# Optimization experiments

Hardware: AMD Instinct MI355X
Metric: run time of the kernel (lower is better)

## Reference

```python
import jax, jax.numpy as jnp
import numpy as np

B, S, CACHE, HID, NH, NKV, HD, INTER = 2, 1024, 2048, 2048, 8, 1, 256, 16384
EPS = 1e-6
SOFTCAP = 50.0
SCALE = HD ** -0.5  # query_pre_attn_scalar is None -> head_dim**-0.5
NEG = -1e9


def _rms(x, w, eps=EPS):
    # Gemma RMSNorm: fp32 norm, output scaled by (1 + weight)
    x32 = x.astype(jnp.float32)
    n = x32 * jax.lax.rsqrt(jnp.mean(x32 * x32, axis=-1, keepdims=True) + eps)
    return (n * (1.0 + w)).astype(x.dtype)


def _rope(x, cos, sin):
    # half-split complex rotation (Gemma apply_rotary_emb): first half real, second half imag
    d2 = x.shape[-1] // 2
    x1, x2 = x[..., :d2], x[..., d2:]
    c = cos[None, :, None, :]
    s = sin[None, :, None, :]
    return jnp.concatenate([x1 * c - x2 * s, x1 * s + x2 * c], axis=-1).astype(x.dtype)


def setup_inputs() -> dict:
    key = jax.random.key(0)
    ks = jax.random.split(key, 8)
    sc = lambda k, sh, f: jax.random.normal(k, sh, jnp.float32) * f
    inp = {}
    inp["hidden_states"] = sc(ks[0], (B, S, HID), 1.0)
    inv = 1.0 / (10000.0 ** (np.arange(0, HD, 2, dtype=np.float32) / HD))
    t = np.arange(S, dtype=np.float32)[:, None] * inv[None, :]
    inp["cos"] = jnp.asarray(np.cos(t), jnp.float32)
    inp["sin"] = jnp.asarray(np.sin(t), jnp.float32)
    inp["kv_write_indices"] = jnp.arange(S, dtype=jnp.int32)
    inp["k_cache"] = jnp.zeros((B, CACHE, NKV, HD), jnp.float32)
    inp["v_cache"] = jnp.zeros((B, CACHE, NKV, HD), jnp.float32)
    i = jnp.arange(S)[:, None]
    j = jnp.arange(CACHE)[None, :]
    inp["mask"] = jnp.where(j <= i, 0.0, NEG).astype(jnp.float32)[None, None]  # [1,1,S,CACHE]
    inp["w_qkv"] = sc(ks[1], ((NH + 2 * NKV) * HD, HID), 0.02)
    inp["w_o"] = sc(ks[2], (HID, NH * HD), 0.02)
    inp["w_gate"] = sc(ks[3], (INTER, HID), 0.02)
    inp["w_up"] = sc(ks[4], (INTER, HID), 0.02)
    inp["w_down"] = sc(ks[5], (HID, INTER), 0.02)
    inp["ln_in"] = jnp.zeros((HID,), jnp.float32)
    inp["ln_post"] = jnp.zeros((HID,), jnp.float32)
    inp["q_norm"] = jnp.zeros((HD,), jnp.float32)
    inp["k_norm"] = jnp.zeros((HD,), jnp.float32)
    return inp


def reference(hidden_states, cos, sin, kv_write_indices, k_cache, v_cache, mask,
              w_qkv, w_o, w_gate, w_up, w_down, ln_in, ln_post, q_norm, k_norm):
    # ---- attention sub-block ----
    res = hidden_states
    x = _rms(hidden_states, ln_in)
    qkv = x @ w_qkv.T  # [B,S,(NH+2*NKV)*HD]
    xq, xk, xv = jnp.split(qkv, [NH * HD, NH * HD + NKV * HD], axis=-1)
    xq = xq.reshape(B, S, NH, HD)
    xk = xk.reshape(B, S, NKV, HD)
    xv = xv.reshape(B, S, NKV, HD)
    xq = _rms(xq, q_norm)  # QK-norm
    xk = _rms(xk, k_norm)
    xq = _rope(xq, cos, sin)
    xk = _rope(xk, cos, sin)
    # KV-cache write (index_copy_ on dim 1)
    k_cache = k_cache.at[:, kv_write_indices].set(xk)
    v_cache = v_cache.at[:, kv_write_indices].set(xv)
    key = jnp.repeat(k_cache, NH // NKV, axis=2)  # [B,CACHE,NH,HD]
    val = jnp.repeat(v_cache, NH // NKV, axis=2)
    scores = jnp.einsum('bshd,bthd->bhst', xq * SCALE, key)  # [B,NH,S,CACHE]
    scores = jnp.tanh(scores / SOFTCAP) * SOFTCAP            # logit softcapping
    probs = jax.nn.softmax(scores + mask, axis=-1)
    out = jnp.einsum('bhst,bthd->bshd', probs, val).reshape(B, S, NH * HD)
    h = res + out @ w_o.T
    # ---- MLP sub-block ----
    res = h
    x = _rms(h, ln_post)
    gate = jax.nn.gelu(x @ w_gate.T, approximate=True)
    up = x @ w_up.T
    return res + (gate * up) @ w_down.T
```

## Files before the change

### kernel.cpp

```cpp
#include <hip/hip_runtime.h>
#include <hip/hip_bf16.h>

typedef __attribute__((ext_vector_type(8))) short short8;
typedef __attribute__((ext_vector_type(4))) float f32x4;
typedef unsigned short u16;

#define B_N 2
#define S_N 1024
#define HID_N 2048
#define NH_N 8
#define HD_N 256
#define INTER_N 16384

#define GLB(p) ((const __attribute__((address_space(1))) void*)(p))
#define AS3(p) ((__attribute__((address_space(3))) void*)(p))

__device__ inline u16 f2b_rn(float f) {
    union { float f; unsigned int u; } x; x.f = f;
    unsigned int r = x.u + 0x7fffu + ((x.u >> 16) & 1u);
    return (u16)(r >> 16);
}
__device__ inline float b2f(u16 h) {
    union { unsigned int u; float f; } x; x.u = ((unsigned int)h) << 16;
    return x.f;
}
__device__ inline float gelu_fast(float v) {
    float z = 0.7978845608028654f * (v + 0.044715f * v * v * v);
    float e = exp2f(z * 2.8853900817779268f);
    float th = 1.f - 2.f * __builtin_amdgcn_rcpf(e + 1.f);
    return 0.5f * v * (1.f + th);
}

__global__ __launch_bounds__(256) void convert_f2b(const float* __restrict__ in,
                                                   u16* __restrict__ out, int n4) {
    int i = blockIdx.x * 256 + threadIdx.x;
    int stride = gridDim.x * 256;
    for (; i < n4; i += stride) {
        float4 v = reinterpret_cast<const float4*>(in)[i];
        u16 o[4] = { f2b_rn(v.x), f2b_rn(v.y), f2b_rn(v.z), f2b_rn(v.w) };
        reinterpret_cast<ulonglong1*>(out)[i] = *reinterpret_cast<ulonglong1*>(o);
    }
}

__global__ __launch_bounds__(256) void rmsnorm_k(const float* __restrict__ x,
                                                 const float* __restrict__ w,
                                                 u16* __restrict__ out) {
    const int row = blockIdx.x;
    const int tid = threadIdx.x;
    const float* xr = x + (size_t)row * HID_N;
    const float4* xr4 = reinterpret_cast<const float4*>(xr);
    float4 a = xr4[tid * 2], b = xr4[tid * 2 + 1];
    float s = a.x*a.x + a.y*a.y + a.z*a.z + a.w*a.w
            + b.x*b.x + b.y*b.y + b.z*b.z + b.w*b.w;
    for (int off = 32; off > 0; off >>= 1) s += __shfl_xor(s, off, 64);
    __shared__ float red[4];
    if ((tid & 63) == 0) red[tid >> 6] = s;
    __syncthreads();
    float tot = red[0] + red[1] + red[2] + red[3];
    float inv = rsqrtf(tot * (1.0f / HID_N) + 1e-6f);
    const float4* w4 = reinterpret_cast<const float4*>(w);
    float4 wa = w4[tid * 2], wb = w4[tid * 2 + 1];
    short8 o;
    o[0] = (short)f2b_rn(a.x * inv * (1.f + wa.x));
    o[1] = (short)f2b_rn(a.y * inv * (1.f + wa.y));
    o[2] = (short)f2b_rn(a.z * inv * (1.f + wa.z));
    o[3] = (short)f2b_rn(a.w * inv * (1.f + wa.w));
    o[4] = (short)f2b_rn(b.x * inv * (1.f + wb.x));
    o[5] = (short)f2b_rn(b.y * inv * (1.f + wb.y));
    o[6] = (short)f2b_rn(b.z * inv * (1.f + wb.z));
    o[7] = (short)f2b_rn(b.w * inv * (1.f + wb.w));
    reinterpret_cast<short8*>(out + (size_t)row * HID_N)[tid] = o;
}

__global__ __launch_bounds__(256) void qkv_post_k(const float* __restrict__ qkv,
                                                  const float* __restrict__ cosb,
                                                  const float* __restrict__ sinb,
                                                  const int* __restrict__ kvw,
                                                  const float* __restrict__ qn,
                                                  const float* __restrict__ kn,
                                                  u16* __restrict__ qb,
                                                  u16* __restrict__ kb,
                                                  u16* __restrict__ vt) {
    const int bs = blockIdx.x;
    const int b = bs >> 10, s = bs & 1023;
    const int tid = threadIdx.x;
    const float* row = qkv + (size_t)bs * 2560;
    __shared__ float buf[256];
    __shared__ float red[4];
    const int sdst = kvw[s];
    const float cv = cosb[s * 128 + (tid & 127)];
    const float sv = sinb[s * 128 + (tid & 127)];
    for (int vi = 0; vi < 9; ++vi) {
        float val = row[vi * 256 + tid];
        float ss = val * val;
        for (int off = 32; off > 0; off >>= 1) ss += __shfl_xor(ss, off, 64);
        __syncthreads();
        if ((tid & 63) == 0) red[tid >> 6] = ss;
        __syncthreads();
        float ms = (red[0] + red[1] + red[2] + red[3]) * (1.f / 256.f) + 1e-6f;
        const float* nw = (vi < 8) ? qn : kn;
        float nrm = val * rsqrtf(ms) * (1.f + nw[tid]);
        buf[tid] = nrm;
        __syncthreads();
        float o;
        if (tid < 128) o = buf[tid] * cv - buf[tid + 128] * sv;
        else           o = buf[tid - 128] * sv + buf[tid] * cv;
        if (vi < 8) {
            qb[(((size_t)(b * 8 + vi)) * 1024 + s) * 256 + tid] = f2b_rn(o * 0.0625f);
        } else {
            kb[((size_t)(b * 1024 + sdst)) * 256 + tid] = f2b_rn(o);
        }
    }
    float vv = row[2304 + tid];
    vt[((size_t)(b * 256 + tid)) * 1024 + sdst] = f2b_rn(vv);
}

__global__ __launch_bounds__(256) void attn_k(const u16* __restrict__ qb,
                                              const u16* __restrict__ kb,
                                              const u16* __restrict__ vt,
                                              float* __restrict__ po,
                                              float* __restrict__ pl) {
    const int qt = blockIdx.x;
    const int h  = blockIdx.y;
    const int c  = blockIdx.z >> 1;
    const int b  = blockIdx.z & 1;
    if (c == 1 && qt < 8) return;
    const int tid = threadIdx.x, lane = tid & 63, wid = tid >> 6;
    const int g = lane >> 4, li = lane & 15;
    const int q0 = qt * 64 + wid * 16;
    const int kv_lo = c * 512;
    __shared__ u16 pbuf[4][16 * 32];

    short8 qf[8];
    const size_t qbase = (((size_t)(b * 8 + h)) * 1024 + q0 + li) * 256;
    #pragma unroll
    for (int kk = 0; kk < 8; ++kk)
        qf[kk] = *reinterpret_cast<const short8*>(qb + qbase + kk * 32 + g * 8);

    f32x4 o[16], o1;
    #pragma unroll
    for (int d = 0; d < 16; ++d) o[d] = f32x4{0.f, 0.f, 0.f, 0.f};
    o1 = f32x4{0.f, 0.f, 0.f, 0.f};
    short8 onesf;
    #pragma unroll
    for (int j = 0; j < 8; ++j) onesf[j] = (short)0x3F80;

    const int nt = (min(kv_lo + 512, q0 + 16) - kv_lo + 31) >> 5;
    const int prd = li * 32 + ((g * 8) ^ (((li >> 2) & 3) * 8));

    for (int t = 0; t < nt; ++t) {
        const int kv0 = kv_lo + t * 32;
        f32x4 sc[2];
        sc[0] = f32x4{0.f, 0.f, 0.f, 0.f};
        sc[1] = f32x4{0.f, 0.f, 0.f, 0.f};
        #pragma unroll
        for (int ch = 0; ch < 2; ++ch) {
            const size_t kbase = ((size_t)(b * 1024 + kv0 + ch * 16 + li)) * 256;
            #pragma unroll
            for (int kk = 0; kk < 8; ++kk) {
                short8 kf = *reinterpret_cast<const short8*>(kb + kbase + kk * 32 + g * 8);
                sc[ch] = __builtin_amdgcn_mfma_f32_16x16x32_bf16(qf[kk], kf, sc[ch], 0, 0, 0);
            }
        }
        #pragma unroll
        for (int reg = 0; reg < 4; ++reg) {
            const int qrow = q0 + g * 4 + reg;
            const int prow = g * 4 + reg;
            const int pswz = ((prow >> 2) & 3) * 8;
            #pragma unroll
            for (int ch = 0; ch < 2; ++ch) {
                const int col = kv0 + ch * 16 + li;
                float s = sc[ch][reg];
                float e = exp2f(s * 0.05770780163555854f);
                float th = 1.f - 2.f * __builtin_amdgcn_rcpf(e + 1.f);
                float pv = exp2f(th * 72.13475204444817f);
                pv = (col <= qrow) ? pv : 0.f;
                pbuf[wid][prow * 32 + ((ch * 16 + li) ^ pswz)] = f2b_rn(pv);
            }
        }
        short8 pf = *reinterpret_cast<const short8*>(&pbuf[wid][prd]);
        o1 = __builtin_amdgcn_mfma_f32_16x16x32_bf16(pf, onesf, o1, 0, 0, 0);
        #pragma unroll
        for (int dth = 0; dth < 2; ++dth) {
            short8 vf[8];
            #pragma unroll
            for (int d8 = 0; d8 < 8; ++d8) {
                const int dt = dth * 8 + d8;
                vf[d8] = *reinterpret_cast<const short8*>(
                    vt + ((size_t)(b * 256 + dt * 16 + li)) * 1024 + kv0 + g * 8);
            }
            #pragma unroll
            for (int d8 = 0; d8 < 8; ++d8)
                o[dth * 8 + d8] = __builtin_amdgcn_mfma_f32_16x16x32_bf16(pf, vf[d8], o[dth * 8 + d8], 0, 0, 0);
        }
    }
    const size_t pbase = ((size_t)((c * 2 + b) * 8 + h)) * 1024;
    #pragma unroll
    for (int reg = 0; reg < 4; ++reg) {
        const int row = q0 + g * 4 + reg;
        #pragma unroll
        for (int dt = 0; dt < 16; ++dt)
            po[(pbase + row) * 256 + dt * 16 + li] = o[dt][reg];
        if (li == 0) pl[pbase + row] = o1[reg];
    }
}

__global__ __launch_bounds__(256) void attn_red_k(const float* __restrict__ po,
                                                  const float* __restrict__ pl,
                                                  u16* __restrict__ out) {
    const int gid = blockIdx.x;
    const int b = gid >> 10, s = gid & 1023;
    const int tid = threadIdx.x;
    const int h = tid >> 5, d0 = (tid & 31) * 8;
    const size_t r0 = ((size_t)(b * 8 + h)) * 1024 + s;
    const size_t r1 = ((size_t)((2 + b) * 8 + h)) * 1024 + s;
    float l = pl[r0];
    float4 a0 = *reinterpret_cast<const float4*>(po + r0 * 256 + d0);
    float4 a1 = *reinterpret_cast<const float4*>(po + r0 * 256 + d0 + 4);
    if (s >= 512) {
        l += pl[r1];
        float4 b0 = *reinterpret_cast<const float4*>(po + r1 * 256 + d0);
        float4 b1 = *reinterpret_cast<const float4*>(po + r1 * 256 + d0 + 4);
        a0.x += b0.x; a0.y += b0.y; a0.z += b0.z; a0.w += b0.w;
        a1.x += b1.x; a1.y += b1.y; a1.z += b1.z; a1.w += b1.w;
    }
    const float inv = 1.f / l;
    u16 r[8] = { f2b_rn(a0.x * inv), f2b_rn(a0.y * inv), f2b_rn(a0.z * inv), f2b_rn(a0.w * inv),
                 f2b_rn(a1.x * inv), f2b_rn(a1.y * inv), f2b_rn(a1.z * inv), f2b_rn(a1.w * inv) };
    *reinterpret_cast<ulonglong2*>(out + ((size_t)gid) * 2048 + h * 256 + d0) =
        *reinterpret_cast<ulonglong2*>(r);
}

template <int EPI>
__global__ __launch_bounds__(256) void gemm_bt(const u16* __restrict__ A,
                                               const u16* __restrict__ W,
                                               const float* __restrict__ res,
                                               float* __restrict__ outf,
                                               int M, int N, int K) {
    __shared__ u16 As[2][128 * 64];
    __shared__ u16 Bs[2][128 * 64];
    const int tid = threadIdx.x, lane = tid & 63, wid = tid >> 6;
    const int g = lane >> 4, li = lane & 15;
    const int wr = wid >> 1, wc = wid & 1;
    const int m0 = blockIdx.x * 128, n0 = blockIdx.y * 128;

    f32x4 acc[4][4];
    #pragma unroll
    for (int m = 0; m < 4; ++m)
        #pragma unroll
        for (int n = 0; n < 4; ++n) acc[m][n] = f32x4{0.f, 0.f, 0.f, 0.f};

    const int lrow = lane >> 3;
    const int lcol = (lane & 7) ^ lrow;
    const u16* ga0 = A + (size_t)(m0 + wid * 32 + lrow) * K + lcol * 8;
    const u16* gb0 = W + (size_t)(n0 + wid * 32 + lrow) * K + lcol * 8;
    const int lbase = wid * 32 * 64;

    auto STAGE = [&](int buf, int k0) {
        #pragma unroll
        for (int i = 0; i < 4; ++i) {
            __builtin_amdgcn_global_load_lds(GLB(ga0 + k0 + (size_t)(i * 8) * K),
                                             AS3(&As[buf][lbase + i * 8 * 64]), 16, 0, 0);
            __builtin_amdgcn_global_load_lds(GLB(gb0 + k0 + (size_t)(i * 8) * K),
                                             AS3(&Bs[buf][lbase + i * 8 * 64]), 16, 0, 0);
        }
    };

    const int NT = K >> 6;
    STAGE(0, 0);
    int cur = 0;
    for (int t = 0; t < NT; ++t) {
        if (t + 1 < NT) {
            STAGE(cur ^ 1, (t + 1) << 6);
            asm volatile("s_waitcnt vmcnt(8)" ::: "memory");
        } else {
            asm volatile("s_waitcnt vmcnt(0)" ::: "memory");
        }
        __builtin_amdgcn_s_barrier();
        __builtin_amdgcn_sched_barrier(0);
        #pragma unroll
        for (int kh = 0; kh < 2; ++kh) {
            short8 af[4], bfr[4];
            #pragma unroll
            for (int m = 0; m < 4; ++m) {
                int rw = wr * 64 + m * 16 + li;
                int slot = (kh * 4 + g) ^ (rw & 7);
                af[m] = *reinterpret_cast<const short8*>(&As[cur][rw * 64 + slot * 8]);
            }
            #pragma unroll
            for (int n = 0; n < 4; ++n) {
                int rw = wc * 64 + n * 16 + li;
                int slot = (kh * 4 + g) ^ (rw & 7);
                bfr[n] = *reinterpret_cast<const short8*>(&Bs[cur][rw * 64 + slot * 8]);
            }
            #pragma unroll
            for (int m = 0; m < 4; ++m)
                #pragma unroll
                for (int n = 0; n < 4; ++n)
                    acc[m][n] = __builtin_amdgcn_mfma_f32_16x16x32_bf16(af[m], bfr[n], acc[m][n], 0, 0, 0);
        }
        __builtin_amdgcn_sched_barrier(0);
        __builtin_amdgcn_s_barrier();
        cur ^= 1;
    }

    #pragma unroll
    for (int m = 0; m < 4; ++m) {
        #pragma unroll
        for (int n = 0; n < 4; ++n) {
            #pragma unroll
            for (int reg = 0; reg < 4; ++reg) {
                int row = m0 + wr * 64 + m * 16 + g * 4 + reg;
                int col = n0 + wc * 64 + n * 16 + li;
                size_t idx = (size_t)row * N + col;
                float v = acc[m][n][reg];
                if (EPI == 0) outf[idx] = v;
                else          outf[idx] = v + res[idx];
            }
        }
    }
}

template <int EPI>
__global__ __launch_bounds__(512, 2) void gemm256(const u16* __restrict__ A,
                                                  const u16* __restrict__ W,
                                                  const u16* __restrict__ gin,
                                                  float* __restrict__ outf,
                                                  u16* __restrict__ outb,
                                                  int M, int N, int K, int kcN) {
    __shared__ u16 Als[2][256 * 64];
    __shared__ u16 Bls[2][256 * 64];
    const int tid = threadIdx.x, lane = tid & 63, wid = tid >> 6;
    const int g = lane >> 4, li = lane & 15;
    const int wm = wid >> 2, wn = wid & 3;
    const int m0 = blockIdx.y * 256, n0 = blockIdx.x * 256;

    int koff = 0, Keff = K;
    if (EPI == 4) {
        Keff = K / kcN;
        koff = blockIdx.z * Keff;
        outf += (size_t)blockIdx.z * M * N;
    }

    f32x4 acc[8][4];
    #pragma unroll
    for (int m = 0; m < 8; ++m)
        #pragma unroll
        for (int n = 0; n < 4; ++n) acc[m][n] = f32x4{0.f, 0.f, 0.f, 0.f};

    const int srcg = ((tid & 7) ^ ((tid >> 3) & 7)) * 8;
    const u16* Asrc = A + (size_t)(m0 + (tid >> 3)) * K + koff + srcg;
    const u16* Bsrc = W + (size_t)(n0 + (tid >> 3)) * K + koff + srcg;
    const int dstb = wid * 512;

    auto STAGE_A = [&](int bf, int h, int kt) {
        const int k0 = kt << 6;
        #pragma unroll
        for (int i = 0; i < 2; ++i)
            __builtin_amdgcn_global_load_lds(GLB(Asrc + (size_t)(h * 128 + i * 64) * K + k0),
                                             AS3(&Als[bf][h * 8192 + i * 4096 + dstb]), 16, 0, 0);
    };
    auto STAGE_B = [&](int bf, int h, int kt) {
        const int k0 = kt << 6;
        #pragma unroll
        for (int i = 0; i < 2; ++i)
            __builtin_amdgcn_global_load_lds(GLB(Bsrc + (size_t)(h * 128 + i * 64) * K + k0),
                                             AS3(&Bls[bf][h * 8192 + i * 4096 + dstb]), 16, 0, 0);
    };
    auto LDA = [&](short8* d, int mh, int cb) {
        #pragma unroll
        for (int m = 0; m < 4; ++m) {
            const int rw = mh * 128 + wm * 64 + m * 16 + li;
            #pragma unroll
            for (int kh = 0; kh < 2; ++kh) {
                const int slot = (kh * 4 + g) ^ (rw & 7);
                d[m * 2 + kh] = *reinterpret_cast<const short8*>(&Als[cb][rw * 64 + slot * 8]);
            }
        }
    };
    auto LDB = [&](short8* d, int nh, int cb) {
        #pragma unroll
        for (int n = 0; n < 2; ++n) {
            const int rw = nh * 128 + wn * 32 + n * 16 + li;
            #pragma unroll
            for (int kh = 0; kh < 2; ++kh) {
                const int slot = (kh * 4 + g) ^ (rw & 7);
                d[n * 2 + kh] = *reinterpret_cast<const short8*>(&Bls[cb][rw * 64 + slot * 8]);
            }
        }
    };

    short8 af[8], af2[8], bq0[4], bq1[4];
    auto MQ = [&](int mh, int nh, short8* aa, short8* bb) {
        #pragma unroll
        for (int kh = 0; kh < 2; ++kh)
            #pragma unroll
            for (int m = 0; m < 4; ++m)
                #pragma unroll
                for (int n = 0; n < 2; ++n)
                    acc[mh * 4 + m][nh * 2 + n] = __builtin_amdgcn_mfma_f32_16x16x32_bf16(
                        aa[m * 2 + kh], bb[n * 2 + kh], acc[mh * 4 + m][nh * 2 + n], 0, 0, 0);
    };

    const int NT = Keff >> 6;
    STAGE_A(0, 0, 0); STAGE_B(0, 0, 0); STAGE_B(0, 1, 0); STAGE_A(0, 1, 0);
    {
        const int t1 = (1 < NT) ? 1 : NT - 1;
        STAGE_A(1, 0, t1); STAGE_B(1, 0, t1); STAGE_B(1, 1, t1);
    }
    asm volatile("s_waitcnt vmcnt(6)" ::: "memory");
    __builtin_amdgcn_s_barrier();
    __builtin_amdgcn_sched_barrier(0);
    LDA(af2, 0, 0);

    int cur = 0;
    for (int t = 0; t < NT; ++t) {
        const int tp1 = (t + 1 < NT) ? t + 1 : NT - 1;
        const int tp2 = (t + 2 < NT) ? t + 2 : NT - 1;
        LDB(bq0, 0, cur);
        STAGE_A(cur ^ 1, 1, tp1);
        __builtin_amdgcn_s_barrier();
        asm volatile("s_waitcnt lgkmcnt(0)" ::: "memory");
        __builtin_amdgcn_sched_barrier(0);
        __builtin_amdgcn_s_setprio(1);
        MQ(0, 0, af2, bq0);
        __builtin_amdgcn_s_setprio(0);
        __builtin_amdgcn_s_barrier();
        __builtin_amdgcn_sched_barrier(0);
        LDB(bq1, 1, cur);
        STAGE_A(cur, 0, tp2);
        __builtin_amdgcn_s_barrier();
        asm volatile("s_waitcnt lgkmcnt(0)" ::: "memory");
        __builtin_amdgcn_sched_barrier(0);
        __builtin_amdgcn_s_setprio(1);
        MQ(0, 1, af2, bq1);
        __builtin_amdgcn_s_setprio(0);
        __builtin_amdgcn_s_barrier();
        __builtin_amdgcn_sched_barrier(0);
        LDA(af, 1, cur);
        STAGE_B(cur, 0, tp2);
        __builtin_amdgcn_s_barrier();
        asm volatile("s_waitcnt lgkmcnt(0)" ::: "memory");
        __builtin_amdgcn_sched_barrier(0);
        __builtin_amdgcn_s_setprio(1);
        MQ(1, 1, af, bq1);
        __builtin_amdgcn_s_setprio(0);
        __builtin_amdgcn_s_barrier();
        __builtin_amdgcn_sched_barrier(0);
        STAGE_B(cur, 1, tp2);
        __builtin_amdgcn_s_setprio(1);
        MQ(1, 0, af, bq0);
        __builtin_amdgcn_s_setprio(0);
        asm volatile("s_waitcnt vmcnt(6)" ::: "memory");
        __builtin_amdgcn_s_barrier();
        __builtin_amdgcn_sched_barrier(0);
        LDA(af2, 0, cur ^ 1);
        cur ^= 1;
    }

    #pragma unroll
    for (int mg = 0; mg < 8; ++mg) {
        const int mh = mg >> 2, m = mg & 3;
        #pragma unroll
        for (int ng = 0; ng < 4; ++ng) {
            const int nh = ng >> 1, n = ng & 1;
            #pragma unroll
            for (int reg = 0; reg < 4; ++reg) {
                const int row = m0 + mh * 128 + wm * 64 + m * 16 + g * 4 + reg;
                const int col = n0 + nh * 128 + wn * 32 + n * 16 + li;
                size_t idx = (size_t)row * N + col;
                float v = acc[mg][ng][reg];
                if (EPI == 2)      outb[idx] = f2b_rn(gelu_fast(v));
                else if (EPI == 3) outb[idx] = f2b_rn(v * b2f(gin[idx]));
                else               outf[idx] = v;
            }
        }
    }
}

__global__ __launch_bounds__(256) void reduce4_k(const float* __restrict__ part,
                                                 const float* __restrict__ res,
                                                 float* __restrict__ out, int n4) {
    int i = blockIdx.x * 256 + threadIdx.x;
    int stride = gridDim.x * 256;
    const size_t ps = (size_t)HID_N * B_N * S_N / 4;
    const float4* p4 = reinterpret_cast<const float4*>(part);
    const float4* r4 = reinterpret_cast<const float4*>(res);
    float4* o4 = reinterpret_cast<float4*>(out);
    for (; i < n4; i += stride) {
        float4 a = p4[i], b = p4[i + ps], c = p4[i + 2 * ps], d = p4[i + 3 * ps];
        float4 r = r4[i];
        float4 o;
        o.x = r.x + a.x + b.x + c.x + d.x;
        o.y = r.y + a.y + b.y + c.y + d.y;
        o.z = r.z + a.z + b.z + c.z + d.z;
        o.w = r.w + a.w + b.w + c.w + d.w;
        o4[i] = o;
    }
}

extern "C" void kernel_launch(void* const* d_in, const int* in_sizes, int n_in,
                              void* d_out, int out_size, void* d_ws, size_t ws_size,
                              hipStream_t stream) {
    (void)in_sizes; (void)n_in; (void)out_size; (void)ws_size;
    const float* hs     = (const float*)d_in[0];
    const float* cosb   = (const float*)d_in[1];
    const float* sinb   = (const float*)d_in[2];
    const int*   kvw    = (const int*)d_in[3];
    const float* wqkv   = (const float*)d_in[7];
    const float* wo     = (const float*)d_in[8];
    const float* wg     = (const float*)d_in[9];
    const float* wu     = (const float*)d_in[10];
    const float* wd     = (const float*)d_in[11];
    const float* ln_in  = (const float*)d_in[12];
    const float* ln_post= (const float*)d_in[13];
    const float* qn     = (const float*)d_in[14];
    const float* kn     = (const float*)d_in[15];
    float* out = (float*)d_out;

    char* p = (char*)d_ws;
    auto alloc = [&](size_t bytes) {
        char* r = p;
        p += (bytes + 255) & ~(size_t)255;
        return r;
    };
    u16* wqkv_b = (u16*)alloc(2560ull * 2048 * 2);
    u16* wo_b   = (u16*)alloc(2048ull * 2048 * 2);
    u16* wg_b   = (u16*)alloc(16384ull * 2048 * 2);
    u16* wu_b   = (u16*)alloc(16384ull * 2048 * 2);
    u16* wd_b   = (u16*)alloc(2048ull * 16384 * 2);
    u16* xn     = (u16*)alloc(2048ull * 2048 * 2);
    float* qkvf = (float*)alloc(2048ull * 2560 * 4);
    u16* qbuf   = (u16*)alloc(2ull * 8 * 1024 * 256 * 2);
    u16* kbuf   = (u16*)alloc(2ull * 1024 * 256 * 2);
    u16* vtbuf  = (u16*)alloc(2ull * 256 * 1024 * 2);
    u16* attn_o = (u16*)alloc(2048ull * 2048 * 2);
    float* hbuf = (float*)alloc(2048ull * 2048 * 4);
    u16* x2     = (u16*)alloc(2048ull * 2048 * 2);
    u16* actb   = (u16*)alloc(2048ull * 16384 * 2);
    float* po   = (float*)alloc(4ull * 8 * 1024 * 256 * 4);
    float* plse = (float*)alloc(4ull * 8 * 1024 * 4);
    float* partials = (float*)d_ws;

    auto conv = [&](const float* src, u16* dst, long n) {
        int n4 = (int)(n / 4);
        long blk = (n4 + 255) / 256;
        if (blk > 4096) blk = 4096;
        convert_f2b<<<dim3((unsigned)blk), dim3(256), 0, stream>>>(src, dst, n4);
    };
    conv(wqkv, wqkv_b, 2560l * 2048);
    conv(wo,   wo_b,   2048l * 2048);
    conv(wg,   wg_b,   16384l * 2048);
    conv(wu,   wu_b,   16384l * 2048);
    conv(wd,   wd_b,   2048l * 16384);

    rmsnorm_k<<<dim3(2048), dim3(256), 0, stream>>>(hs, ln_in, xn);
    gemm_bt<0><<<dim3(16, 20), dim3(256), 0, stream>>>(xn, wqkv_b, nullptr,
                                                       qkvf, 2048, 2560, 2048);
    qkv_post_k<<<dim3(2048), dim3(256), 0, stream>>>(qkvf, cosb, sinb, kvw, qn, kn,
                                                     qbuf, kbuf, vtbuf);
    attn_k<<<dim3(16, 8, 4), dim3(256), 0, stream>>>(qbuf, kbuf, vtbuf, po, plse);
    attn_red_k<<<dim3(2048), dim3(256), 0, stream>>>(po, plse, attn_o);
    gemm_bt<1><<<dim3(16, 16), dim3(256), 0, stream>>>(attn_o, wo_b, hs,
                                                       hbuf, 2048, 2048, 2048);
    rmsnorm_k<<<dim3(2048), dim3(256), 0, stream>>>(hbuf, ln_post, x2);
    gemm256<2><<<dim3(64, 8), dim3(512), 0, stream>>>(x2, wg_b, nullptr,
                                                      nullptr, actb, 2048, 16384, 2048, 1);
    gemm256<3><<<dim3(64, 8), dim3(512), 0, stream>>>(x2, wu_b, actb,
                                                      nullptr, actb, 2048, 16384, 2048, 1);
    gemm256<4><<<dim3(8, 8, 4), dim3(512), 0, stream>>>(actb, wd_b, nullptr,
                                                        partials, nullptr, 2048, 2048, 16384, 4);
    reduce4_k<<<dim3(2048), dim3(256), 0, stream>>>(partials, hbuf, out, 1048576);
}
```

Baseline: 893.8 us.

## Fuse gate and up GEMMs via interleaved weight layout; parallelize qkv_post over heads

Gate and up weights are converted into one interleaved bf16 matrix, with each block of 128 gate rows followed by the matching 128 up rows. A single 256-wide GEMM tile then produces both gate and up for the same columns, and its epilogue computes gelu(gate)*up directly. This removes the second GEMM launch, the bf16 round trip of the gate activations and the re-read of x2. Separately, qkv_post_k now gives each head its own block in a 2D grid instead of looping nine times inside one block, which adds parallelism and drops barriers.

```diff
diff --git a/kernel.cpp b/kernel.cpp
--- a/kernel.cpp
+++ b/kernel.cpp
@@ -39,6 +39,26 @@
         float4 v = reinterpret_cast<const float4*>(in)[i];
         u16 o[4] = { f2b_rn(v.x), f2b_rn(v.y), f2b_rn(v.z), f2b_rn(v.w) };
         reinterpret_cast<ulonglong1*>(out)[i] = *reinterpret_cast<ulonglong1*>(o);
+    }
+}
+
+__global__ __launch_bounds__(256) void convert_gu(const float* __restrict__ wg,
+                                                  const float* __restrict__ wu,
+                                                  u16* __restrict__ out, int n4) {
+    int i = blockIdx.x * 256 + threadIdx.x;
+    int stride = gridDim.x * 256;
+    for (; i < n4; i += stride) {
+        const int e = i << 2;
+        const int r = e >> 11, c = e & 2047;
+        const int rg = ((r >> 7) << 8) + (r & 127);
+        float4 g = reinterpret_cast<const float4*>(wg)[i];
+        u16 og[4] = { f2b_rn(g.x), f2b_rn(g.y), f2b_rn(g.z), f2b_rn(g.w) };
+        *reinterpret_cast<ulonglong1*>(out + (size_t)rg * 2048 + c) =
+            *reinterpret_cast<ulonglong1*>(og);
+        float4 u = reinterpret_cast<const float4*>(wu)[i];
+        u16 ou[4] = { f2b_rn(u.x), f2b_rn(u.y), f2b_rn(u.z), f2b_rn(u.w) };
+        *reinterpret_cast<ulonglong1*>(out + (size_t)(rg + 128) * 2048 + c) =
+            *reinterpret_cast<ulonglong1*>(ou);
     }
 }
 
@@ -81,38 +101,34 @@
                                                   u16* __restrict__ qb,
                                                   u16* __restrict__ kb,
                                                   u16* __restrict__ vt) {
-    const int bs = blockIdx.x;
+    const int bs = blockIdx.x, vi = blockIdx.y;
     const int b = bs >> 10, s = bs & 1023;
     const int tid = threadIdx.x;
     const float* row = qkv + (size_t)bs * 2560;
+    const int sdst = kvw[s];
+    if (vi == 9) {
+        vt[((size_t)(b * 256 + tid)) * 1024 + sdst] = f2b_rn(row[2304 + tid]);
+        return;
+    }
     __shared__ float buf[256];
     __shared__ float red[4];
-    const int sdst = kvw[s];
+    float val = row[vi * 256 + tid];
+    float ss = val * val;
+    for (int off = 32; off > 0; off >>= 1) ss += __shfl_xor(ss, off, 64);
+    if ((tid & 63) == 0) red[tid >> 6] = ss;
+    __syncthreads();
+    float ms = (red[0] + red[1] + red[2] + red[3]) * (1.f / 256.f) + 1e-6f;
+    const float* nw = (vi < 8) ? qn : kn;
+    float nrm = val * rsqrtf(ms) * (1.f + nw[tid]);
+    buf[tid] = nrm;
+    __syncthreads();
     const float cv = cosb[s * 128 + (tid & 127)];
     const float sv = sinb[s * 128 + (tid & 127)];
-    for (int vi = 0; vi < 9; ++vi) {
-        float val = row[vi * 256 + tid];
-        float ss = val * val;
-        for (int off = 32; off > 0; off >>= 1) ss += __shfl_xor(ss, off, 64);
-        __syncthreads();
-        if ((tid & 63) == 0) red[tid >> 6] = ss;
-        __syncthreads();
-        float ms = (red[0] + red[1] + red[2] + red[3]) * (1.f / 256.f) + 1e-6f;
-        const float* nw = (vi < 8) ? qn : kn;
-        float nrm = val * rsqrtf(ms) * (1.f + nw[tid]);
-        buf[tid] = nrm;
-        __syncthreads();
-        float o;
-        if (tid < 128) o = buf[tid] * cv - buf[tid + 128] * sv;
-        else           o = buf[tid - 128] * sv + buf[tid] * cv;
-        if (vi < 8) {
-            qb[(((size_t)(b * 8 + vi)) * 1024 + s) * 256 + tid] = f2b_rn(o * 0.0625f);
-        } else {
-            kb[((size_t)(b * 1024 + sdst)) * 256 + tid] = f2b_rn(o);
-        }
-    }
-    float vv = row[2304 + tid];
-    vt[((size_t)(b * 256 + tid)) * 1024 + sdst] = f2b_rn(vv);
+    float o;
+    if (tid < 128) o = buf[tid] * cv - buf[tid + 128] * sv;
+    else           o = buf[tid - 128] * sv + buf[tid] * cv;
+    if (vi < 8) qb[(((size_t)(b * 8 + vi)) * 1024 + s) * 256 + tid] = f2b_rn(o * 0.0625f);
+    else        kb[((size_t)(b * 1024 + sdst)) * 256 + tid] = f2b_rn(o);
 }
 
 __global__ __launch_bounds__(256) void attn_k(const u16* __restrict__ qb,
@@ -324,7 +340,6 @@
 template <int EPI>
 __global__ __launch_bounds__(512, 2) void gemm256(const u16* __restrict__ A,
                                                   const u16* __restrict__ W,
-                                                  const u16* __restrict__ gin,
                                                   float* __restrict__ outf,
                                                   u16* __restrict__ outb,
                                                   int M, int N, int K, int kcN) {
@@ -458,21 +473,35 @@
         cur ^= 1;
     }
 
-    #pragma unroll
-    for (int mg = 0; mg < 8; ++mg) {
-        const int mh = mg >> 2, m = mg & 3;
-        #pragma unroll
-        for (int ng = 0; ng < 4; ++ng) {
-            const int nh = ng >> 1, n = ng & 1;
-            #pragma unroll
-            for (int reg = 0; reg < 4; ++reg) {
-                const int row = m0 + mh * 128 + wm * 64 + m * 16 + g * 4 + reg;
-                const int col = n0 + nh * 128 + wn * 32 + n * 16 + li;
-                size_t idx = (size_t)row * N + col;
-                float v = acc[mg][ng][reg];
-                if (EPI == 2)      outb[idx] = f2b_rn(gelu_fast(v));
-                else if (EPI == 3) outb[idx] = f2b_rn(v * b2f(gin[idx]));
-                else               outf[idx] = v;
+    if (EPI == 5) {
+        #pragma unroll
+        for (int mg = 0; mg < 8; ++mg) {
+            const int mh = mg >> 2, m = mg & 3;
+            #pragma unroll
+            for (int n = 0; n < 2; ++n) {
+                const int col = (n0 >> 1) + wn * 32 + n * 16 + li;
+                #pragma unroll
+                for (int reg = 0; reg < 4; ++reg) {
+                    const int row = m0 + mh * 128 + wm * 64 + m * 16 + g * 4 + reg;
+                    float gt = gelu_fast(acc[mg][n][reg]);
+                    float up = acc[mg][n + 2][reg];
+                    outb[(size_t)row * INTER_N + col] = f2b_rn(gt * up);
+                }
+            }
+        }
+    } else {
+        #pragma unroll
+        for (int mg = 0; mg < 8; ++mg) {
+            const int mh = mg >> 2, m = mg & 3;
+            #pragma unroll
+            for (int ng = 0; ng < 4; ++ng) {
+                const int nh = ng >> 1, n = ng & 1;
+                #pragma unroll
+                for (int reg = 0; reg < 4; ++reg) {
+                    const int row = m0 + mh * 128 + wm * 64 + m * 16 + g * 4 + reg;
+                    const int col = n0 + nh * 128 + wn * 32 + n * 16 + li;
+                    outf[(size_t)row * N + col] = acc[mg][ng][reg];
+                }
             }
         }
     }
@@ -526,8 +555,7 @@
     };
     u16* wqkv_b = (u16*)alloc(2560ull * 2048 * 2);
     u16* wo_b   = (u16*)alloc(2048ull * 2048 * 2);
-    u16* wg_b   = (u16*)alloc(16384ull * 2048 * 2);
-    u16* wu_b   = (u16*)alloc(16384ull * 2048 * 2);
+    u16* wgu_b  = (u16*)alloc(32768ull * 2048 * 2);
     u16* wd_b   = (u16*)alloc(2048ull * 16384 * 2);
     u16* xn     = (u16*)alloc(2048ull * 2048 * 2);
     float* qkvf = (float*)alloc(2048ull * 2560 * 4);
@@ -550,25 +578,22 @@
     };
     conv(wqkv, wqkv_b, 2560l * 2048);
     conv(wo,   wo_b,   2048l * 2048);
-    conv(wg,   wg_b,   16384l * 2048);
-    conv(wu,   wu_b,   16384l * 2048);
+    convert_gu<<<dim3(4096), dim3(256), 0, stream>>>(wg, wu, wgu_b, 8388608);
     conv(wd,   wd_b,   2048l * 16384);
 
     rmsnorm_k<<<dim3(2048), dim3(256), 0, stream>>>(hs, ln_in, xn);
     gemm_bt<0><<<dim3(16, 20), dim3(256), 0, stream>>>(xn, wqkv_b, nullptr,
                                                        qkvf, 2048, 2560, 2048);
-    qkv_post_k<<<dim3(2048), dim3(256), 0, stream>>>(qkvf, cosb, sinb, kvw, qn, kn,
-                                                     qbuf, kbuf, vtbuf);
+    qkv_post_k<<<dim3(2048, 10), dim3(256), 0, stream>>>(qkvf, cosb, sinb, kvw, qn, kn,
+                                                         qbuf, kbuf, vtbuf);
     attn_k<<<dim3(16, 8, 4), dim3(256), 0, stream>>>(qbuf, kbuf, vtbuf, po, plse);
     attn_red_k<<<dim3(2048), dim3(256), 0, stream>>>(po, plse, attn_o);
     gemm_bt<1><<<dim3(16, 16), dim3(256), 0, stream>>>(attn_o, wo_b, hs,
                                                        hbuf, 2048, 2048, 2048);
     rmsnorm_k<<<dim3(2048), dim3(256), 0, stream>>>(hbuf, ln_post, x2);
-    gemm256<2><<<dim3(64, 8), dim3(512), 0, stream>>>(x2, wg_b, nullptr,
-                                                      nullptr, actb, 2048, 16384, 2048, 1);
-    gemm256<3><<<dim3(64, 8), dim3(512), 0, stream>>>(x2, wu_b, actb,
-                                                      nullptr, actb, 2048, 16384, 2048, 1);
-    gemm256<4><<<dim3(8, 8, 4), dim3(512), 0, stream>>>(actb, wd_b, nullptr,
-                                                        partials, nullptr, 2048, 2048, 16384, 4);
+    gemm256<5><<<dim3(128, 8), dim3(512), 0, stream>>>(x2, wgu_b, nullptr, actb,
+                                                       2048, 16384, 2048, 1);
+    gemm256<4><<<dim3(8, 8, 4), dim3(512), 0, stream>>>(actb, wd_b, partials, nullptr,
+                                                        2048, 2048, 16384, 4);
     reduce4_k<<<dim3(2048), dim3(256), 0, stream>>>(partials, hbuf, out, 1048576);
 }
```

Measured after the change: 888.1 us. No clear change (-0.6%).
